# Kernel optimization log

Hardware: AMD Instinct MI355X
Metric: run time of the kernel (lower is better)

## Reference

```python
import jax, jax.numpy as jnp
import numpy as np

DIM = 2048
STATE = 2048
SEL_H = 1024
B = 16384


def setup_inputs() -> dict:
    key = jax.random.key(0)
    ks = jax.random.split(key, 7)
    def lin(k, out_f, in_f):
        return jax.random.normal(k, (out_f, in_f), dtype=jnp.float32) / np.sqrt(in_f)
    return {
        "x_t": jax.random.normal(ks[0], (B, DIM), dtype=jnp.float32),
        "h_prev": jax.random.normal(ks[1], (B, STATE), dtype=jnp.float32),
        "W_in": lin(ks[2], STATE, DIM),
        "W_sel_in": lin(ks[3], SEL_H, DIM),
        "W_sel_out": lin(ks[4], 4 * STATE, SEL_H),
        "W_out": lin(ks[5], DIM, STATE),
        "d": jnp.ones((STATE,), dtype=jnp.float32),
    }


def reference(x_t, h_prev, W_in, W_sel_in, W_sel_out, W_out, d):
    # u_t = in_proj(x_t): [B, state]
    u_t = x_t @ W_in.T
    # selector: silu(x @ W_sel_in.T) @ W_sel_out.T -> [B, 4*state]
    sel_h = jax.nn.silu(x_t @ W_sel_in.T)
    sel = sel_h @ W_sel_out.T
    a_raw, b_raw, c_raw, d_raw = jnp.split(sel, 4, axis=-1)
    a_t = jax.nn.sigmoid(a_raw)
    b_t = jnp.tanh(b_raw)
    c_t = jnp.tanh(c_raw)
    d_t = jax.nn.sigmoid(d_raw)
    h_t = a_t * h_prev + b_t * u_t
    y_t = c_t * h_t + d[None, :] * d_t * u_t
    out = y_t @ W_out.T  # [B, dim]
    return (out, h_t)
```

## Files before the change

kernel.cpp:

```cpp
#include <hip/hip_runtime.h>
#include <hip/hip_bf16.h>
#include <cstdint>

#define NB    16384
#define DIMX  2048
#define STATE 2048
#define SELH  1024

typedef unsigned short u16;
typedef short  short8_t __attribute__((ext_vector_type(8)));
typedef float  f32x4    __attribute__((ext_vector_type(4)));

__device__ __forceinline__ u16 f2bf(float f) {
  unsigned u = __builtin_bit_cast(unsigned, f);
  u += 0x7fffu + ((u >> 16) & 1u);
  return (u16)(u >> 16);
}
__device__ __forceinline__ float bf2f(u16 h) {
  unsigned u = ((unsigned)h) << 16;
  return __builtin_bit_cast(float, u);
}
__device__ __forceinline__ float sigmoidf_(float x) { return 1.f / (1.f + __expf(-x)); }
__device__ __forceinline__ float tanhf_(float x)    { return 2.f / (1.f + __expf(-2.f * x)) - 1.f; }

__device__ __forceinline__ f32x4 mfma_bf16(short8_t a, short8_t b, f32x4 c) {
  return __builtin_amdgcn_mfma_f32_16x16x32_bf16(a, b, c, 0, 0, 0);
}

__device__ __forceinline__ void gload16(const void* g, const void* l) {
  __builtin_amdgcn_global_load_lds(
      (const __attribute__((address_space(1))) unsigned int*)(uintptr_t)g,
      (__attribute__((address_space(3))) unsigned int*)(unsigned int)(uintptr_t)l,
      16, 0, 0);
}

#define LDS_V(p) (*(const short8_t*)__builtin_assume_aligned((const void*)(p), 16))

__global__ __launch_bounds__(256) void k_f32_to_bf16(const float* __restrict__ src,
                                                     u16* __restrict__ dst, int n4) {
  int i = blockIdx.x * blockDim.x + threadIdx.x;
  int stride = gridDim.x * blockDim.x;
  for (; i < n4; i += stride) {
    float4 v = ((const float4*)src)[i];
    ushort4 o;
    o.x = f2bf(v.x); o.y = f2bf(v.y); o.z = f2bf(v.z); o.w = f2bf(v.w);
    ((ushort4*)dst)[i] = o;
  }
}

template <int EPI, int KD, int NCOLS>
__global__ __launch_bounds__(512, 2) void k_gemm256(const u16* __restrict__ A,
                                                    const u16* __restrict__ Bsrc,
                                                    float* __restrict__ f32out,
                                                    u16* __restrict__ bfout,
                                                    const float* __restrict__ hprev,
                                                    const u16* __restrict__ ubf,
                                                    const float* __restrict__ dvec) {
  __shared__ __align__(16) char smem[131072];
  const int tid = threadIdx.x;
  const int w = tid >> 6, l = tid & 63;
  const int wr = w >> 2, wc = w & 3;
  const int bx = blockIdx.x, by = blockIdx.y;
  const int m0 = by * 256;

  const unsigned aAddr0 = (unsigned)(wr * 16384 + (l & 15) * 128 +
                                     (((l >> 4) * 16) ^ ((l & 7) << 4)));
  const unsigned aAddr1 = aAddr0 ^ 64u;
  const unsigned bAddr0 = (unsigned)(65536 + (wc * 64 + (l & 15)) * 64 +
                                     (((l >> 4) * 16) ^ ((l & 3) << 4)));
  const unsigned bAddr1 = bAddr0 + 16384u;

  const int rA = tid >> 3;
  const int kA = ((tid & 7) ^ ((tid >> 3) & 7)) * 8;
  const u16* aSrc = A + (size_t)(m0 + rA) * KD + kA;

  const int rB = tid >> 2;
  const int kB = ((tid & 3) ^ ((tid >> 2) & 3)) * 8;
  size_t bRow0, bRow1;
  if constexpr (EPI <= 2) {
    bRow0 = (size_t)bx * 256 + rB;
    bRow1 = bRow0 + 128;
  } else {
    const int s0 = bx * 64;
    const int r1 = rB + 128;
    bRow0 = (size_t)((rB >> 4) & 3) * STATE + s0 + (rB >> 6) * 16 + (rB & 15);
    bRow1 = (size_t)((r1 >> 4) & 3) * STATE + s0 + (r1 >> 6) * 16 + (r1 & 15);
  }
  const u16* bSrc0 = Bsrc + bRow0 * KD + kB;
  const u16* bSrc1 = Bsrc + bRow1 * KD + kB;

  auto stageA = [&](int k0n, int rh, unsigned dstD) {
    const u16* sp = aSrc + (size_t)rh * 128 * KD + k0n;
    gload16(sp,           smem + dstD + (unsigned)rh * 16384u + (unsigned)tid * 16u);
    gload16(sp + 64 * KD, smem + dstD + (unsigned)rh * 16384u + 8192u + (unsigned)tid * 16u);
  };
  auto stageB = [&](int k0n, int kh, unsigned dstD) {
    const int kk = k0n + kh * 32;
    gload16(bSrc0 + kk, smem + 65536u + dstD + (unsigned)kh * 16384u + (unsigned)tid * 16u);
    gload16(bSrc1 + kk, smem + 65536u + dstD + (unsigned)kh * 16384u + 8192u + (unsigned)tid * 16u);
  };

  f32x4 acc[8][4];
#pragma unroll
  for (int i = 0; i < 8; ++i)
#pragma unroll
    for (int j = 0; j < 4; ++j) acc[i][j] = f32x4{0.f, 0.f, 0.f, 0.f};

  short8_t av[8], bvN[2], bvM[2];

#define LOAD_AV(D, KK)                                                         \
  _Pragma("unroll") for (int mf = 0; mf < 8; ++mf)                             \
      av[mf] = LDS_V(smem + ((KK) ? aAddr1 : aAddr0) + (D) * 32768u + mf * 2048u);
#define LOAD_BV(R, I, NF, D, KK)                                               \
  R[I] = LDS_V(smem + ((KK) ? bAddr1 : bAddr0) + (D) * 32768u + (NF) * 1024u);
#define MFMA8x2(BV, NFA, NFB)                                                  \
  __builtin_amdgcn_s_setprio(1);                                               \
  _Pragma("unroll") for (int mf = 0; mf < 8; ++mf) {                           \
    acc[mf][NFA] = mfma_bf16(av[mf], BV[0], acc[mf][NFA]);                     \
    acc[mf][NFB] = mfma_bf16(av[mf], BV[1], acc[mf][NFB]);                     \
  }                                                                            \
  __builtin_amdgcn_s_setprio(0);

#define KTILE(D, K0, DO_STAGE, K0N, LASTT)                                     \
  {                                                                            \
                                                           \
    LOAD_AV(D, 0);                                                             \
    LOAD_BV(bvN, 0, 0, D, 0); LOAD_BV(bvN, 1, 1, D, 0);                        \
    if (DO_STAGE) stageA(K0N, 0, (D ^ 1) * 32768u);                            \
    __builtin_amdgcn_s_barrier();                                              \
    MFMA8x2(bvN, 0, 1);                                                        \
    __builtin_amdgcn_s_barrier();                                              \
                                                           \
    LOAD_BV(bvM, 0, 2, D, 0); LOAD_BV(bvM, 1, 3, D, 0);                        \
    if (DO_STAGE) stageA(K0N, 1, (D ^ 1) * 32768u);                            \
    if (LASTT) { asm volatile("s_waitcnt vmcnt(0)" ::: "memory"); }            \
    else       { asm volatile("s_waitcnt vmcnt(4)" ::: "memory"); }            \
    __builtin_amdgcn_s_barrier();                                              \
    MFMA8x2(bvM, 2, 3);                                                        \
    __builtin_amdgcn_s_barrier();                                              \
                                                           \
    LOAD_AV(D, 1);                                                             \
    LOAD_BV(bvM, 0, 2, D, 1); LOAD_BV(bvM, 1, 3, D, 1);                        \
    if (DO_STAGE) stageB(K0N, 0, (D ^ 1) * 32768u);                            \
    __builtin_amdgcn_s_barrier();                                              \
    MFMA8x2(bvM, 2, 3);                                                        \
    __builtin_amdgcn_s_barrier();                                              \
                                                           \
    LOAD_BV(bvN, 0, 0, D, 1); LOAD_BV(bvN, 1, 1, D, 1);                        \
    if (DO_STAGE) stageB(K0N, 1, (D ^ 1) * 32768u);                            \
    if (!LASTT) { asm volatile("s_waitcnt vmcnt(2)" ::: "memory"); }           \
    __builtin_amdgcn_s_barrier();                                              \
    MFMA8x2(bvN, 0, 1);                                                        \
    __builtin_amdgcn_s_barrier();                                              \
  }

  stageA(0, 0, 0u); stageA(0, 1, 0u); stageB(0, 0, 0u); stageB(0, 1, 0u);
  asm volatile("s_waitcnt vmcnt(2)" ::: "memory");
  __builtin_amdgcn_s_barrier();

  constexpr int NT = KD / 64;
  int k0 = 0;
#pragma unroll 1
  for (int T = 0; T < NT - 2; T += 2) {
    KTILE(0, k0, true, k0 + 64, false);
    KTILE(1, k0 + 64, true, k0 + 128, false);
    k0 += 128;
  }
  KTILE(0, k0, true, k0 + 64, false);
  KTILE(1, k0 + 64, false, 0, true);

#undef KTILE
#undef MFMA8x2
#undef LOAD_BV
#undef LOAD_AV

  const int rbase = m0 + wr * 128 + ((l >> 4) << 2);
  if constexpr (EPI <= 2) {
    const int cbase = bx * 256 + wc * 64 + (l & 15);
#pragma unroll
    for (int mf = 0; mf < 8; ++mf)
#pragma unroll
      for (int nf = 0; nf < 4; ++nf)
#pragma unroll
        for (int r = 0; r < 4; ++r) {
          const int row = rbase + mf * 16 + r;
          const int col = cbase + nf * 16;
          const size_t idx = (size_t)row * NCOLS + col;
          const float v = acc[mf][nf][r];
          if constexpr (EPI == 0) {
            bfout[idx] = f2bf(v);
          } else if constexpr (EPI == 1) {
            bfout[idx] = f2bf(v * sigmoidf_(v));
          } else {
            f32out[idx] = v;
          }
        }
  } else {
    const int s = bx * 64 + wc * 16 + (l & 15);
    const float dval = dvec[s];
#pragma unroll
    for (int mf = 0; mf < 8; ++mf)
#pragma unroll
      for (int r = 0; r < 4; ++r) {
        const int row = rbase + mf * 16 + r;
        const size_t idx = (size_t)row * STATE + s;
        const float a  = acc[mf][0][r];
        const float b  = acc[mf][1][r];
        const float c  = acc[mf][2][r];
        const float dd = acc[mf][3][r];
        const float uu = bf2f(ubf[idx]);
        const float hp = hprev[idx];
        const float h = sigmoidf_(a) * hp + tanhf_(b) * uu;
        f32out[idx] = h;
        bfout[idx] = f2bf(tanhf_(c) * h + dval * sigmoidf_(dd) * uu);
      }
  }
}

extern "C" void kernel_launch(void* const* d_in, const int* in_sizes, int n_in,
                              void* d_out, int out_size, void* d_ws, size_t ws_size,
                              hipStream_t stream) {
  const float* x   = (const float*)d_in[0];
  const float* h0  = (const float*)d_in[1];
  const float* Win = (const float*)d_in[2];
  const float* Wsi = (const float*)d_in[3];
  const float* Wso = (const float*)d_in[4];
  const float* Wou = (const float*)d_in[5];
  const float* dv  = (const float*)d_in[6];
  float* out  = (float*)d_out;
  float* hout = out + (size_t)NB * DIMX;

  u16* ws = (u16*)d_ws;
  size_t o = 0;
  u16* xb   = ws + o; o += (size_t)NB * DIMX;
  u16* ub   = ws + o; o += (size_t)NB * STATE;
  u16* yb   = ws + o; o += (size_t)NB * STATE;
  u16* sh   = ws + o; o += (size_t)NB * SELH;
  u16* wib  = ws + o; o += (size_t)STATE * DIMX;
  u16* wsib = ws + o; o += (size_t)SELH * DIMX;
  u16* wsob = ws + o; o += (size_t)4 * STATE * SELH;
  u16* wob  = ws + o; o += (size_t)DIMX * STATE;

  k_f32_to_bf16<<<1024, 256, 0, stream>>>(x,   xb,   NB * DIMX / 4);
  k_f32_to_bf16<<<256,  256, 0, stream>>>(Win, wib,  STATE * DIMX / 4);
  k_f32_to_bf16<<<128,  256, 0, stream>>>(Wsi, wsib, SELH * DIMX / 4);
  k_f32_to_bf16<<<512,  256, 0, stream>>>(Wso, wsob, 4 * STATE * SELH / 4);
  k_f32_to_bf16<<<256,  256, 0, stream>>>(Wou, wob,  DIMX * STATE / 4);

  const dim3 blk(512);
  k_gemm256<0, DIMX, STATE><<<dim3(STATE / 256, NB / 256), blk, 0, stream>>>(
      xb, wib, nullptr, ub, nullptr, nullptr, nullptr);
  k_gemm256<1, DIMX, SELH><<<dim3(SELH / 256, NB / 256), blk, 0, stream>>>(
      xb, wsib, nullptr, sh, nullptr, nullptr, nullptr);
  k_gemm256<3, SELH, 0><<<dim3(STATE / 64, NB / 256), blk, 0, stream>>>(
      sh, wsob, hout, yb, h0, ub, dv);
  k_gemm256<2, STATE, DIMX><<<dim3(DIMX / 256, NB / 256), blk, 0, stream>>>(
      yb, wob, out, nullptr, nullptr, nullptr, nullptr);
}
```

Baseline: 798.2 us.

## Restructure GEMM K-tile pipeline to use two barriers per tile

Rewrites the inner K-tile macro of the bf16 MFMA GEMM. It drops from eight workgroup barriers per tile to two, and issues both A-half and B-half global stages together. The two K-halves now get separate A-fragment registers (ava/avb), so LDS reads for the second half can be issued ahead of the MFMAs that use the first half. sched_barrier pins the instruction order. The aim is to cut barrier stalls and let LDS reads and global loads overlap more with MFMA work, at the cost of more live VGPRs and a tighter vmcnt-based synchronisation scheme that must stay correct.

```diff
diff --git a/kernel.cpp b/kernel.cpp
--- a/kernel.cpp
+++ b/kernel.cpp
@@ -106,73 +106,78 @@
 #pragma unroll
     for (int j = 0; j < 4; ++j) acc[i][j] = f32x4{0.f, 0.f, 0.f, 0.f};
 
-  short8_t av[8], bvN[2], bvM[2];
-
-#define LOAD_AV(D, KK)                                                         \
-  _Pragma("unroll") for (int mf = 0; mf < 8; ++mf)                             \
-      av[mf] = LDS_V(smem + ((KK) ? aAddr1 : aAddr0) + (D) * 32768u + mf * 2048u);
-#define LOAD_BV(R, I, NF, D, KK)                                               \
-  R[I] = LDS_V(smem + ((KK) ? bAddr1 : bAddr0) + (D) * 32768u + (NF) * 1024u);
-#define MFMA8x2(BV, NFA, NFB)                                                  \
-  __builtin_amdgcn_s_setprio(1);                                               \
-  _Pragma("unroll") for (int mf = 0; mf < 8; ++mf) {                           \
-    acc[mf][NFA] = mfma_bf16(av[mf], BV[0], acc[mf][NFA]);                     \
-    acc[mf][NFB] = mfma_bf16(av[mf], BV[1], acc[mf][NFB]);                     \
-  }                                                                            \
-  __builtin_amdgcn_s_setprio(0);
-
-#define KTILE(D, K0, DO_STAGE, K0N, LASTT)                                     \
+  short8_t ava[8], avb[8], bv01a[2], bv23a[2], bv23b[2], bv01b[2];
+
+#define KTILE(D, DO_STAGE, K0N, LASTT)                                         \
   {                                                                            \
-                                                           \
-    LOAD_AV(D, 0);                                                             \
-    LOAD_BV(bvN, 0, 0, D, 0); LOAD_BV(bvN, 1, 1, D, 0);                        \
-    if (DO_STAGE) stageA(K0N, 0, (D ^ 1) * 32768u);                            \
+                                                        \
+    if (LASTT) { asm volatile("s_waitcnt vmcnt(0)" ::: "memory"); }            \
+    else       { asm volatile("s_waitcnt vmcnt(2)" ::: "memory"); }            \
     __builtin_amdgcn_s_barrier();                                              \
-    MFMA8x2(bvN, 0, 1);                                                        \
-    __builtin_amdgcn_s_barrier();                                              \
-                                                           \
-    LOAD_BV(bvM, 0, 2, D, 0); LOAD_BV(bvM, 1, 3, D, 0);                        \
-    if (DO_STAGE) stageA(K0N, 1, (D ^ 1) * 32768u);                            \
+    __builtin_amdgcn_sched_barrier(0);                                         \
+    bv01a[0] = LDS_V(smem + bAddr0 + (D) * 32768u);                            \
+    bv01a[1] = LDS_V(smem + bAddr0 + (D) * 32768u + 1024u);                    \
+    _Pragma("unroll") for (int mf = 0; mf < 8; ++mf)                           \
+        ava[mf] = LDS_V(smem + aAddr0 + (D) * 32768u + mf * 2048u);            \
+    if (DO_STAGE) { stageA(K0N, 0, (D ^ 1) * 32768u);                          \
+                    stageA(K0N, 1, (D ^ 1) * 32768u); }                        \
+    __builtin_amdgcn_s_setprio(1);                                             \
+    _Pragma("unroll") for (int mf = 0; mf < 8; ++mf) {                         \
+      acc[mf][0] = mfma_bf16(ava[mf], bv01a[0], acc[mf][0]);                   \
+      acc[mf][1] = mfma_bf16(ava[mf], bv01a[1], acc[mf][1]);                   \
+    }                                                                          \
+    __builtin_amdgcn_s_setprio(0);                                             \
+                                                                       \
     if (LASTT) { asm volatile("s_waitcnt vmcnt(0)" ::: "memory"); }            \
     else       { asm volatile("s_waitcnt vmcnt(4)" ::: "memory"); }            \
     __builtin_amdgcn_s_barrier();                                              \
-    MFMA8x2(bvM, 2, 3);                                                        \
-    __builtin_amdgcn_s_barrier();                                              \
-                                                           \
-    LOAD_AV(D, 1);                                                             \
-    LOAD_BV(bvM, 0, 2, D, 1); LOAD_BV(bvM, 1, 3, D, 1);                        \
-    if (DO_STAGE) stageB(K0N, 0, (D ^ 1) * 32768u);                            \
-    __builtin_amdgcn_s_barrier();                                              \
-    MFMA8x2(bvM, 2, 3);                                                        \
-    __builtin_amdgcn_s_barrier();                                              \
-                                                           \
-    LOAD_BV(bvN, 0, 0, D, 1); LOAD_BV(bvN, 1, 1, D, 1);                        \
-    if (DO_STAGE) stageB(K0N, 1, (D ^ 1) * 32768u);                            \
-    if (!LASTT) { asm volatile("s_waitcnt vmcnt(2)" ::: "memory"); }           \
-    __builtin_amdgcn_s_barrier();                                              \
-    MFMA8x2(bvN, 0, 1);                                                        \
-    __builtin_amdgcn_s_barrier();                                              \
+    __builtin_amdgcn_sched_barrier(0);                                         \
+    bv23a[0] = LDS_V(smem + bAddr0 + (D) * 32768u + 2048u);                    \
+    bv23a[1] = LDS_V(smem + bAddr0 + (D) * 32768u + 3072u);                    \
+    bv23b[0] = LDS_V(smem + bAddr1 + (D) * 32768u + 2048u);                    \
+    bv23b[1] = LDS_V(smem + bAddr1 + (D) * 32768u + 3072u);                    \
+    _Pragma("unroll") for (int mf = 0; mf < 8; ++mf)                           \
+        avb[mf] = LDS_V(smem + aAddr1 + (D) * 32768u + mf * 2048u);            \
+    if (DO_STAGE) { stageB(K0N, 0, (D ^ 1) * 32768u);                          \
+                    stageB(K0N, 1, (D ^ 1) * 32768u); }                        \
+    __builtin_amdgcn_s_setprio(1);                                             \
+    _Pragma("unroll") for (int mf = 0; mf < 8; ++mf) {                         \
+      acc[mf][2] = mfma_bf16(ava[mf], bv23a[0], acc[mf][2]);                   \
+      acc[mf][3] = mfma_bf16(ava[mf], bv23a[1], acc[mf][3]);                   \
+    }                                                                          \
+    __builtin_amdgcn_s_setprio(0);                                             \
+                                                          \
+    bv01b[0] = LDS_V(smem + bAddr1 + (D) * 32768u);                            \
+    bv01b[1] = LDS_V(smem + bAddr1 + (D) * 32768u + 1024u);                    \
+    __builtin_amdgcn_s_setprio(1);                                             \
+    _Pragma("unroll") for (int mf = 0; mf < 8; ++mf) {                         \
+      acc[mf][2] = mfma_bf16(avb[mf], bv23b[0], acc[mf][2]);                   \
+      acc[mf][3] = mfma_bf16(avb[mf], bv23b[1], acc[mf][3]);                   \
+    }                                                                          \
+    __builtin_amdgcn_s_setprio(0);                                             \
+                                                          \
+    __builtin_amdgcn_s_setprio(1);                                             \
+    _Pragma("unroll") for (int mf = 0; mf < 8; ++mf) {                         \
+      acc[mf][0] = mfma_bf16(avb[mf], bv01b[0], acc[mf][0]);                   \
+      acc[mf][1] = mfma_bf16(avb[mf], bv01b[1], acc[mf][1]);                   \
+    }                                                                          \
+    __builtin_amdgcn_s_setprio(0);                                             \
   }
 
   stageA(0, 0, 0u); stageA(0, 1, 0u); stageB(0, 0, 0u); stageB(0, 1, 0u);
-  asm volatile("s_waitcnt vmcnt(2)" ::: "memory");
-  __builtin_amdgcn_s_barrier();
 
   constexpr int NT = KD / 64;
   int k0 = 0;
 #pragma unroll 1
   for (int T = 0; T < NT - 2; T += 2) {
-    KTILE(0, k0, true, k0 + 64, false);
-    KTILE(1, k0 + 64, true, k0 + 128, false);
+    KTILE(0, true, k0 + 64, false);
+    KTILE(1, true, k0 + 128, false);
     k0 += 128;
   }
-  KTILE(0, k0, true, k0 + 64, false);
-  KTILE(1, k0 + 64, false, 0, true);
+  KTILE(0, true, k0 + 64, false);
+  KTILE(1, false, 0, true);
 
 #undef KTILE
-#undef MFMA8x2
-#undef LOAD_BV
-#undef LOAD_AV
 
   const int rbase = m0 + wr * 128 + ((l >> 4) << 2);
   if constexpr (EPI <= 2) {
```

Result: faster. 755.7 us (-5.3%).

## Restructure MFMA phases to 4x4 quadrants with B fragments reused across halves

Applied to the files above, without the earlier changes.

Reorganizes each K-tile's inner loop from 8x2 MFMA blocks into 4x4 blocks over M-halves. The four B fragments per K-subtile are loaded once and reused for both M halves, and A fragments are loaded four at a time. Each phase now ends with an explicit lgkmcnt(0) wait and a sched_barrier. The intent is to cut register pressure for A fragments and to make LDS-read and MFMA interleaving more predictable, at the cost of stricter scheduling constraints and an extra wait per phase.

```diff
diff --git a/kernel.cpp b/kernel.cpp
--- a/kernel.cpp
+++ b/kernel.cpp
@@ -106,52 +106,55 @@
 #pragma unroll
     for (int j = 0; j < 4; ++j) acc[i][j] = f32x4{0.f, 0.f, 0.f, 0.f};
 
-  short8_t av[8], bvN[2], bvM[2];
-
-#define LOAD_AV(D, KK)                                                         \
-  _Pragma("unroll") for (int mf = 0; mf < 8; ++mf)                             \
-      av[mf] = LDS_V(smem + ((KK) ? aAddr1 : aAddr0) + (D) * 32768u + mf * 2048u);
-#define LOAD_BV(R, I, NF, D, KK)                                               \
-  R[I] = LDS_V(smem + ((KK) ? bAddr1 : bAddr0) + (D) * 32768u + (NF) * 1024u);
-#define MFMA8x2(BV, NFA, NFB)                                                  \
-  __builtin_amdgcn_s_setprio(1);                                               \
-  _Pragma("unroll") for (int mf = 0; mf < 8; ++mf) {                           \
-    acc[mf][NFA] = mfma_bf16(av[mf], BV[0], acc[mf][NFA]);                     \
-    acc[mf][NFB] = mfma_bf16(av[mf], BV[1], acc[mf][NFB]);                     \
-  }                                                                            \
-  __builtin_amdgcn_s_setprio(0);
-
-#define KTILE(D, K0, DO_STAGE, K0N, LASTT)                                     \
+  short8_t avq[4], bk0[4], bk1[4];
+
+#define PH_TAIL()                                                              \
+    __builtin_amdgcn_s_barrier();                                              \
+    asm volatile("s_waitcnt lgkmcnt(0)" ::: "memory");                         \
+    __builtin_amdgcn_sched_barrier(0);
+
+#define MFMA16(MBASE, BK)                                                      \
+    __builtin_amdgcn_s_setprio(1);                                             \
+    _Pragma("unroll") for (int mf = 0; mf < 4; ++mf)                           \
+      _Pragma("unroll") for (int nf = 0; nf < 4; ++nf)                         \
+        acc[(MBASE) + mf][nf] = mfma_bf16(avq[mf], BK[nf],                     \
+                                          acc[(MBASE) + mf][nf]);              \
+    __builtin_amdgcn_s_setprio(0);                                             \
+    __builtin_amdgcn_s_barrier();
+
+#define KTILE(D, DO_STAGE, K0N, LASTT)                                         \
   {                                                                            \
-                                                           \
-    LOAD_AV(D, 0);                                                             \
-    LOAD_BV(bvN, 0, 0, D, 0); LOAD_BV(bvN, 1, 1, D, 0);                        \
+                                                   \
+    _Pragma("unroll") for (int mf = 0; mf < 4; ++mf)                           \
+        avq[mf] = LDS_V(smem + aAddr0 + (D) * 32768u + mf * 2048u);            \
+    _Pragma("unroll") for (int nf = 0; nf < 4; ++nf)                           \
+        bk0[nf] = LDS_V(smem + bAddr0 + (D) * 32768u + nf * 1024u);            \
     if (DO_STAGE) stageA(K0N, 0, (D ^ 1) * 32768u);                            \
-    __builtin_amdgcn_s_barrier();                                              \
-    MFMA8x2(bvN, 0, 1);                                                        \
-    __builtin_amdgcn_s_barrier();                                              \
-                                                           \
-    LOAD_BV(bvM, 0, 2, D, 0); LOAD_BV(bvM, 1, 3, D, 0);                        \
+    PH_TAIL();                                                                 \
+    MFMA16(0, bk0);                                                            \
+                                                   \
+    _Pragma("unroll") for (int mf = 0; mf < 4; ++mf)                           \
+        avq[mf] = LDS_V(smem + aAddr0 + (D) * 32768u + (mf + 4) * 2048u);      \
     if (DO_STAGE) stageA(K0N, 1, (D ^ 1) * 32768u);                            \
     if (LASTT) { asm volatile("s_waitcnt vmcnt(0)" ::: "memory"); }            \
     else       { asm volatile("s_waitcnt vmcnt(4)" ::: "memory"); }            \
-    __builtin_amdgcn_s_barrier();                                              \
-    MFMA8x2(bvM, 2, 3);                                                        \
-    __builtin_amdgcn_s_barrier();                                              \
-                                                           \
-    LOAD_AV(D, 1);                                                             \
-    LOAD_BV(bvM, 0, 2, D, 1); LOAD_BV(bvM, 1, 3, D, 1);                        \
+    PH_TAIL();                                                                 \
+    MFMA16(4, bk0);                                                            \
+                                                   \
+    _Pragma("unroll") for (int mf = 0; mf < 4; ++mf)                           \
+        avq[mf] = LDS_V(smem + aAddr1 + (D) * 32768u + mf * 2048u);            \
+    _Pragma("unroll") for (int nf = 0; nf < 4; ++nf)                           \
+        bk1[nf] = LDS_V(smem + bAddr1 + (D) * 32768u + nf * 1024u);            \
     if (DO_STAGE) stageB(K0N, 0, (D ^ 1) * 32768u);                            \
-    __builtin_amdgcn_s_barrier();                                              \
-    MFMA8x2(bvM, 2, 3);                                                        \
-    __builtin_amdgcn_s_barrier();                                              \
-                                                           \
-    LOAD_BV(bvN, 0, 0, D, 1); LOAD_BV(bvN, 1, 1, D, 1);                        \
+    PH_TAIL();                                                                 \
+    MFMA16(0, bk1);                                                            \
+                                                   \
+    _Pragma("unroll") for (int mf = 0; mf < 4; ++mf)                           \
+        avq[mf] = LDS_V(smem + aAddr1 + (D) * 32768u + (mf + 4) * 2048u);      \
     if (DO_STAGE) stageB(K0N, 1, (D ^ 1) * 32768u);                            \
     if (!LASTT) { asm volatile("s_waitcnt vmcnt(2)" ::: "memory"); }           \
-    __builtin_amdgcn_s_barrier();                                              \
-    MFMA8x2(bvN, 0, 1);                                                        \
-    __builtin_amdgcn_s_barrier();                                              \
+    PH_TAIL();                                                                 \
+    MFMA16(4, bk1);                                                            \
   }
 
   stageA(0, 0, 0u); stageA(0, 1, 0u); stageB(0, 0, 0u); stageB(0, 1, 0u);
@@ -162,17 +165,16 @@
   int k0 = 0;
 #pragma unroll 1
   for (int T = 0; T < NT - 2; T += 2) {
-    KTILE(0, k0, true, k0 + 64, false);
-    KTILE(1, k0 + 64, true, k0 + 128, false);
+    KTILE(0, true, k0 + 64, false);
+    KTILE(1, true, k0 + 128, false);
     k0 += 128;
   }
-  KTILE(0, k0, true, k0 + 64, false);
-  KTILE(1, k0 + 64, false, 0, true);
+  KTILE(0, true, k0 + 64, false);
+  KTILE(1, false, 0, true);
 
 #undef KTILE
-#undef MFMA8x2
-#undef LOAD_BV
-#undef LOAD_AV
+#undef MFMA16
+#undef PH_TAIL
 
   const int rbase = m0 + wr * 128 + ((l >> 4) << 2);
   if constexpr (EPI <= 2) {
```

Measured after the change: 800.2 us. No clear change (+0.2%).
